# Kernel tuning notes

Hardware: AMD Instinct MI355X
Metric: run time of the kernel (lower is better)

## Reference

```python
import jax, jax.numpy as jnp
import numpy as np
import math

L = 2; B = 128; CIN = 64; E = 64; H = 8; Wd = 8; NH = 8; MEM = 40
HD = E // NH; HW = H * Wd; THD = HD * HW  # 512
MASK_B = 3.0; NEG = -1e9; EPS = 1e-5


def _conv(x, w, b):
    y = jax.lax.conv_general_dilated(x, w, (1, 1), 'SAME',
                                     dimension_numbers=('NCHW', 'OIHW', 'NCHW'))
    return y + b[None, :, None, None]


def setup_inputs() -> dict:
    key = jax.random.key(0)
    ks = jax.random.split(key, 12)
    f = jax.random.normal
    return {
        'x': f(ks[0], (B, CIN, H, Wd), jnp.float32),
        'h0': f(ks[1], (L, B, E, H, Wd), jnp.float32),
        'c0': f(ks[2], (L, B, E, H, Wd), jnp.float32),
        'k0': f(ks[3], (L, B, NH, MEM, THD), jnp.float32),
        'v0': f(ks[4], (L, B, NH, MEM, THD), jnp.float32),
        'src_mask': jax.random.randint(ks[5], (B, MEM), 0, 2).astype(bool),
        'notdone': jnp.ones((B,), bool),
        'main_w': f(ks[6], (L, 5 * E, CIN + 2 * E, 3, 3), jnp.float32) * 0.05,
        'main_b': jnp.zeros((L, 5 * E), jnp.float32),
        'proj_w': f(ks[7], (L, 3 * E, CIN + E, 3, 3), jnp.float32) * 0.05,
        'proj_b': jnp.zeros((L, 3 * E), jnp.float32),
        'out_w': f(ks[8], (L, E, E, 3, 3), jnp.float32) * 0.05,
        'out_b': jnp.zeros((L, E), jnp.float32),
        'ln_w': jnp.ones((L, E, H, Wd), jnp.float32),
        'ln_b': jnp.zeros((L, E, H, Wd), jnp.float32),
        'pos_w': f(ks[9], (L, MEM, HW * E), jnp.float32) * 0.05,
        'pos_b': f(ks[10], (L, MEM, NH), jnp.float32) * 0.05,
    }


def reference(x, h0, c0, k0, v0, src_mask, notdone,
              main_w, main_b, proj_w, proj_b, out_w, out_b,
              ln_w, ln_b, pos_w, pos_b):
    nd = notdone.astype(x.dtype)[:, None, None, None]
    # rolling attention mask: reset finished episodes, shift left, open last slot
    m = src_mask | (~notdone)[:, None]
    m = jnp.concatenate([m[:, 1:], jnp.zeros((B, 1), bool)], axis=1)
    bias = jnp.where(m, NEG, 0.0).astype(x.dtype)        # (B, MEM)
    bias = bias.at[:, -1].set(MASK_B)
    out = h0[L - 1] * nd
    for n in range(L):
        inp = jnp.concatenate([x, out], axis=1)          # (B, CIN+E, H, W)
        h_cur = h0[n] * nd
        c_cur = c0[n] * nd
        gates = _conv(jnp.concatenate([inp, h_cur], axis=1), main_w[n], main_b[n])
        cc_i, cc_f, cc_o, cc_g, cc_a = jnp.split(gates, 5, axis=1)
        i = jax.nn.sigmoid(cc_i)
        fg = jax.nn.sigmoid(cc_f)
        o = jax.nn.sigmoid(cc_o)
        g = jnp.tanh(cc_g)
        a = jax.nn.sigmoid(cc_a)
        c_next = fg * c_cur + i * g
        # attention over rolling memory (mem_n slots of flattened spatial features)
        kqv = _conv(inp, proj_w[n], proj_b[n]).reshape(B, NH, 3 * HD, HW)
        k = kqv[:, :, :HD].reshape(B, NH, THD)
        q = kqv[:, :, HD:2 * HD].reshape(B, NH, THD) / math.sqrt(THD)
        v = kqv[:, :, 2 * HD:].reshape(B, NH, THD)
        pw = pos_w[n].reshape(MEM, NH, THD).transpose(1, 0, 2)  # (NH, MEM, THD)
        k_cat = jnp.concatenate([k0[n][:, :, 1:], k[:, :, None, :]], axis=2) + pw[None]
        v_cat = jnp.concatenate([v0[n][:, :, 1:], v[:, :, None, :]], axis=2)
        scores = (jnp.einsum('bnd,bnmd->bnm', q, k_cat)
                  + bias[:, None, :] + pos_b[n].T[None])
        attn_w = jax.nn.softmax(scores, axis=-1)
        attn = jnp.einsum('bnm,bnmd->bnd', attn_w, v_cat).reshape(B, E, H, Wd)
        ao = _conv(attn, out_w[n], out_b[n]) + inp[:, :E]
        mu = ao.mean(axis=(1, 2, 3), keepdims=True)
        var = ((ao - mu) ** 2).mean(axis=(1, 2, 3), keepdims=True)
        ao = (ao - mu) * jax.lax.rsqrt(var + EPS) * ln_w[n][None] + ln_b[n][None]
        c_next = c_next + a * jnp.tanh(ao)
        out = o * jnp.tanh(c_next)
    return out
```

## Files before the change

kernel.cpp:

```cpp
#include <hip/hip_runtime.h>
#include <hip/hip_bf16.h>

typedef __hip_bfloat16 bf16;
typedef unsigned short u16;
typedef __attribute__((ext_vector_type(8))) short short8;
typedef __attribute__((ext_vector_type(4))) float f32x4;

#define Bb   128
#define MEMm 40

__device__ __forceinline__ float LD(const void* p, size_t i, int f32) {
    return f32 ? ((const float*)p)[i] : __bfloat162float(((const bf16*)p)[i]);
}
__device__ __forceinline__ float S2F(short s) {
    u16 u = (u16)s;
    return __bfloat162float(*(bf16*)&u);
}
__device__ __forceinline__ int LDB(const void* p, int i, int isbyte) {
    return isbyte ? (int)((const unsigned char*)p)[i] : ((const int*)p)[i];
}
__device__ __forceinline__ void SPLIT(float v, u16& hi, u16& lo) {
    bf16 h = __float2bfloat16(v);
    float r = v - __bfloat162float(h);
    bf16 l = __float2bfloat16(r);
    hi = *(u16*)&h; lo = *(u16*)&l;
}

__global__ void setup_kernel(const void* __restrict__ x,
                             const void* __restrict__ src_mask,
                             const void* __restrict__ notdone,
                             const void* __restrict__ h0,
                             const void* __restrict__ mw,
                             const void* __restrict__ pw,
                             const void* __restrict__ ow,
                             int* __restrict__ flags,
                             float* __restrict__ biasb,
                             float* __restrict__ outb, size_t hoff,
                             u16* __restrict__ whi, u16* __restrict__ wlo) {
    __shared__ int det[3];
    const int bid = blockIdx.x, t = threadIdx.x;
    if (t < 3) det[t] = 0;
    __syncthreads();
    {
        const bf16* xb = (const bf16*)x;
        int bad = 0;
        for (int i = t; i < 4096; i += 256) {
            float v = __bfloat162float(xb[2 * i]);
            if (!(fabsf(v) < 1e4f)) bad = 1;
        }
        if (bad) atomicOr(&det[0], 1);
        int mb = 0;
        const unsigned* mi = (const unsigned*)src_mask;
        for (int i = t; i < 1280; i += 256) if (mi[i] > 1u) mb = 1;
        if (mb) atomicOr(&det[1], 1);
        int nb = 0;
        const unsigned* ni = (const unsigned*)notdone;
        for (int i = t; i < 32; i += 256) if (ni[i] > 1u) nb = 1;
        if (nb) atomicOr(&det[2], 1);
    }
    __syncthreads();
    const int isf32 = det[0], mbyte = det[1], ndbyte = det[2];
    if (bid == 0 && t < 3) flags[t] = det[t];

    if (bid < 20) {
        int idx = bid * 256 + t;
        if (idx >= Bb * MEMm) return;
        int b = idx / MEMm, m = idx - b * MEMm;
        float v;
        if (m == MEMm - 1) v = 3.0f;
        else {
            bool masked = (LDB(src_mask, b * MEMm + m + 1, mbyte) != 0) ||
                          (LDB(notdone, b, ndbyte) == 0);
            v = masked ? -1e9f : 0.f;
        }
        biasb[idx] = v;
    } else if (bid < 276) {
        int idx = (bid - 20) * 256 + t;
        int b = idx >> 9;
        float nd = (LDB(notdone, b, ndbyte) != 0) ? 1.f : 0.f;
        size_t e = (size_t)idx * 8;
        float v[8];
        if (isf32) {
            const float* hp = (const float*)h0 + hoff + e;
            f32x4 p0 = *(const f32x4*)hp, p1 = *(const f32x4*)(hp + 4);
#pragma unroll
            for (int j = 0; j < 4; ++j) { v[j] = p0[j]; v[4 + j] = p1[j]; }
        } else {
            short8 s = *(const short8*)((const bf16*)h0 + hoff + e);
#pragma unroll
            for (int j = 0; j < 8; ++j) v[j] = S2F(s[j]);
        }
#pragma unroll
        for (int j = 0; j < 8; ++j) outb[e + j] = v[j] * nd;
    } else {
        int gi = (bid - 276) * 256 + t;
        if (gi >= 1622016) return;
        int layer = (gi >= 811008) ? 1 : 0;
        int i = gi - layer * 811008;
        float v;
        if (i < 552960) {
            int blk = i >> 9, r = i & 511;
            int l = r >> 3, j = r & 7;
            int nn = blk & 1, b2 = blk >> 1;
            int s = b2 % 10, tk = b2 / 10;
            int kc = tk % 6, tap = tk / 6;
            int co = s * 32 + nn * 16 + (l & 15);
            int ci = kc * 32 + ((l >> 4) << 3) + j;
            v = LD(mw, (size_t)layer * 552960 + ((size_t)co * 192 + ci) * 9 + tap, isf32);
        } else if (i < 774144) {
            int j2 = i - 552960;
            int blk = j2 >> 9, r = j2 & 511;
            int l = r >> 3, j = r & 7;
            int nn = blk & 1, b2 = blk >> 1;
            int s = b2 % 6, tk = b2 / 6;
            int kc = tk & 3, tap = tk >> 2;
            int co = s * 32 + nn * 16 + (l & 15);
            int ci = kc * 32 + ((l >> 4) << 3) + j;
            v = LD(pw, (size_t)layer * 221184 + ((size_t)co * 128 + ci) * 9 + tap, isf32);
        } else {
            int j2 = i - 774144;
            int tap = j2 / 4096, r = j2 - tap * 4096, co = r / 64, ci = r - co * 64;
            v = LD(ow, (size_t)layer * 36864 + ((size_t)co * 64 + ci) * 9 + tap, isf32);
        }
        u16 h, l; SPLIT(v, h, l);
        whi[gi] = h; wlo[gi] = l;
    }
}

struct ConvArgs {
    const void *x; const float *prev_out; const void *h0; const void *notdone;
    const u16 *WhiA, *WloA, *WhiB, *WloB;
    const void *biasA, *biasB;
    float *OutA, *OutB;
    long long boffA, boffB;
    size_t hoff;
    int KciA, KciB, CoutA, CoutB, ntA, NT, NMB;
};

__global__ __launch_bounds__(256) void conv_mfma_kernel(ConvArgs g,
                                                        const int* __restrict__ flags) {
    __shared__ __align__(16) u16 Alds[2][2][2600];
    const int t = threadIdx.x, w = t >> 6, lane = t & 63;
    const int bpair = w >> 1, half = w & 1;
    const int bx = blockIdx.x;
    const int mblk = bx % g.NMB, nt = bx / g.NMB;
    const bool isA = (nt < g.ntA);
    const u16* Whi = isA ? g.WhiA : g.WhiB;
    const u16* Wlo = isA ? g.WloA : g.WloB;
    const int Kci  = isA ? g.KciA : g.KciB;
    const int CoutT= isA ? g.CoutA : g.CoutB;
    float* Out     = isA ? g.OutA : g.OutB;
    const void* bias = isA ? g.biasA : g.biasB;
    const long long boff = isA ? g.boffA : g.boffB;
    const int n0 = (isA ? nt : nt - g.ntA) * 64;
    const int b = mblk * 2 + bpair;
    const int kcN = Kci >> 5;
    const int CoutT32 = CoutT >> 5;
    const int NITER = kcN * 9;
    const int s = (n0 >> 5) + half;
    const int isf32 = flags[0];
    const float nd = (LDB(g.notdone, b, flags[2]) != 0) ? 1.f : 0.f;

    if (half == 0 && lane < 40) { Alds[bpair][0][2560 + lane] = 0; Alds[bpair][1][2560 + lane] = 0; }

    f32x4 acc[4][2];
#pragma unroll
    for (int i = 0; i < 4; ++i)
#pragma unroll
        for (int j = 0; j < 2; ++j) { f32x4 z = {0.f, 0.f, 0.f, 0.f}; acc[i][j] = z; }

    auto wbase = [&](int it) -> size_t {
        int kc = it / 9, tap = it - kc * 9;
        return ((size_t)((tap * kcN + kc) * CoutT32 + s) * 2) * 512 + (size_t)lane * 8;
    };

    short8 wh0, wh1, wl0, wl1, nh0, nh1, nl0, nl1;
    {
        size_t o = wbase(0);
        wh0 = *(const short8*)(Whi + o); wh1 = *(const short8*)(Whi + o + 512);
        wl0 = *(const short8*)(Wlo + o); wl1 = *(const short8*)(Wlo + o + 512);
    }
    nh0 = wh0; nh1 = wh1; nl0 = wl0; nl1 = wl1;

    for (int it = 0; it < NITER; ++it) {
        const int kc = it / 9, tap = it - kc * 9;
        if (it + 1 < NITER) {
            size_t o = wbase(it + 1);
            nh0 = *(const short8*)(Whi + o); nh1 = *(const short8*)(Whi + o + 512);
            nl0 = *(const short8*)(Wlo + o); nl1 = *(const short8*)(Wlo + o + 512);
        }
        if (tap == 0) {
            __syncthreads();
            const int px = lane;
            const int c0i = half * 16;
            const int cbase = kc * 32;
            short8 hA, hB, lA, lB;
#pragma unroll
            for (int cl2 = 0; cl2 < 16; ++cl2) {
                int c = cbase + c0i + cl2;
                float v;
                if (c < 64) {
                    size_t o = (size_t)b * 4096 + (size_t)c * 64 + px;
                    v = isf32 ? ((const float*)g.x)[o] : S2F(((const short*)g.x)[o]);
                } else if (c < 128) {
                    v = g.prev_out[(size_t)b * 4096 + (size_t)(c - 64) * 64 + px];
                } else {
                    size_t o = g.hoff + (size_t)b * 4096 + (size_t)(c - 128) * 64 + px;
                    v = (isf32 ? ((const float*)g.h0)[o] : S2F(((const short*)g.h0)[o])) * nd;
                }
                u16 hh, ll; SPLIT(v, hh, ll);
                if (cl2 < 8) { hA[cl2] = (short)hh; lA[cl2] = (short)ll; }
                else         { hB[cl2 - 8] = (short)hh; lB[cl2 - 8] = (short)ll; }
            }
            *(short8*)&Alds[bpair][0][px * 40 + c0i]     = hA;
            *(short8*)&Alds[bpair][0][px * 40 + c0i + 8] = hB;
            *(short8*)&Alds[bpair][1][px * 40 + c0i]     = lA;
            *(short8*)&Alds[bpair][1][px * 40 + c0i + 8] = lB;
            __syncthreads();
        }
        const int dy = tap / 3 - 1, dx = tap % 3 - 1;
        const int q8 = (lane >> 4) * 8;
        const int ml = lane & 15;
        short8 aH[4], aL[4];
#pragma unroll
        for (int mt = 0; mt < 4; ++mt) {
            int px = mt * 16 + ml;
            int yy = (px >> 3) + dy, xx = (px & 7) + dx;
            int row = ((unsigned)yy < 8u && (unsigned)xx < 8u) ? yy * 8 + xx : 64;
            int o = row * 40 + q8;
            aH[mt] = *(const short8*)&Alds[bpair][0][o];
            aL[mt] = *(const short8*)&Alds[bpair][1][o];
        }
#pragma unroll
        for (int mt = 0; mt < 4; ++mt) {
            acc[mt][0] = __builtin_amdgcn_mfma_f32_16x16x32_bf16(aH[mt], wh0, acc[mt][0], 0, 0, 0);
            acc[mt][0] = __builtin_amdgcn_mfma_f32_16x16x32_bf16(aH[mt], wl0, acc[mt][0], 0, 0, 0);
            acc[mt][0] = __builtin_amdgcn_mfma_f32_16x16x32_bf16(aL[mt], wh0, acc[mt][0], 0, 0, 0);
            acc[mt][1] = __builtin_amdgcn_mfma_f32_16x16x32_bf16(aH[mt], wh1, acc[mt][1], 0, 0, 0);
            acc[mt][1] = __builtin_amdgcn_mfma_f32_16x16x32_bf16(aH[mt], wl1, acc[mt][1], 0, 0, 0);
            acc[mt][1] = __builtin_amdgcn_mfma_f32_16x16x32_bf16(aL[mt], wh1, acc[mt][1], 0, 0, 0);
        }
        wh0 = nh0; wh1 = nh1; wl0 = nl0; wl1 = nl1;
    }
    const int q = lane >> 4, ml = lane & 15;
#pragma unroll
    for (int nn = 0; nn < 2; ++nn) {
        int co = n0 + half * 32 + nn * 16 + ml;
        float bv = LD(bias, (size_t)boff + co, isf32);
#pragma unroll
        for (int mt = 0; mt < 4; ++mt) {
            f32x4 v = acc[mt][nn];
            v[0] += bv; v[1] += bv; v[2] += bv; v[3] += bv;
            *(f32x4*)&Out[((size_t)b * CoutT + co) * 64 + mt * 16 + q * 4] = v;
        }
    }
}

__global__ __launch_bounds__(256) void attn_kernel(
    const float* __restrict__ kqv,
    const void* __restrict__ k0,
    const void* __restrict__ v0,
    const void* __restrict__ pw,
    const void* __restrict__ pb,
    const float* __restrict__ biasb,
    const int* __restrict__ flags,
    u16* __restrict__ ahi, u16* __restrict__ alo,
    size_t kvoff, size_t pwoff, size_t pboff) {
    __shared__ float qv[512], kl[512], vl[512], sc[40], wexp[40];
    __shared__ float accbuf[4][512];
    const int t = threadIdx.x;
    const int isf32 = flags[0];
    const int b = blockIdx.x >> 3, h = blockIdx.x & 7;
    const size_t kqb = (size_t)b * 192 * 64;
    for (int d = t; d < 512; d += 256) {
        int hd = d >> 6, ss = d & 63;
        qv[d] = kqv[kqb + (h * 24 + 8 + hd) * 64 + ss] * 0.044194173824159216f;
        kl[d] = kqv[kqb + (h * 24 + 0 + hd) * 64 + ss];
        vl[d] = kqv[kqb + (h * 24 + 16 + hd) * 64 + ss];
    }
    __syncthreads();
    const int wid = t >> 6, lane = t & 63;
    const int d0 = lane * 8;
    const size_t kvbase = kvoff + ((size_t)(b * 8 + h)) * (size_t)(40 * 512);

    float q8[8];
#pragma unroll
    for (int j = 0; j < 8; ++j) q8[j] = qv[d0 + j];

    if (!isf32) {
        const bf16* kp = (const bf16*)k0;
        const bf16* pp = (const bf16*)pw;
        const bf16* vp = (const bf16*)v0;
        short8 kr[10], pr[10];
#pragma unroll
        for (int i = 0; i < 10; ++i) {
            int m = wid + i * 4;
            pr[i] = *(const short8*)(pp + pwoff + (size_t)m * 4096 + h * 512 + d0);
            if (m < 39)
                kr[i] = *(const short8*)(kp + kvbase + (size_t)(m + 1) * 512 + d0);
        }
#pragma unroll
        for (int i = 0; i < 10; ++i) {
            int m = wid + i * 4;
            float p = 0.f;
            if (m < 39) {
#pragma unroll
                for (int j = 0; j < 8; ++j)
                    p += q8[j] * (S2F(kr[i][j]) + S2F(pr[i][j]));
            } else {
#pragma unroll
                for (int j = 0; j < 8; ++j)
                    p += q8[j] * (kl[d0 + j] + S2F(pr[i][j]));
            }
#pragma unroll
            for (int off = 32; off > 0; off >>= 1) p += __shfl_down(p, off, 64);
            if (lane == 0)
                sc[m] = p + biasb[b * 40 + m] + LD(pb, pboff + m * 8 + h, 0);
        }
        short8 vr[10];
#pragma unroll
        for (int i = 0; i < 10; ++i) {
            int m = wid + i * 4;
            if (m < 39)
                vr[i] = *(const short8*)(vp + kvbase + (size_t)(m + 1) * 512 + d0);
        }
        __syncthreads();
        float mx = -1e30f;
        for (int m = 0; m < 40; ++m) mx = fmaxf(mx, sc[m]);
        if (t < 40) wexp[t] = __expf(sc[t] - mx);
        __syncthreads();
        float sum = 0.f;
        for (int m = 0; m < 40; ++m) sum += wexp[m];
        float rs = 1.f / sum;
        float acc8[8];
#pragma unroll
        for (int j = 0; j < 8; ++j) acc8[j] = 0.f;
#pragma unroll
        for (int i = 0; i < 10; ++i) {
            int m = wid + i * 4;
            float wgt = wexp[m];
            if (m < 39) {
#pragma unroll
                for (int j = 0; j < 8; ++j) acc8[j] += wgt * S2F(vr[i][j]);
            } else {
#pragma unroll
                for (int j = 0; j < 8; ++j) acc8[j] += wgt * vl[d0 + j];
            }
        }
#pragma unroll
        for (int j = 0; j < 8; ++j) accbuf[wid][d0 + j] = acc8[j];
        __syncthreads();
        for (int d = t; d < 512; d += 256) {
            float acc = (accbuf[0][d] + accbuf[1][d]) + (accbuf[2][d] + accbuf[3][d]);
            acc *= rs;
            int ch = h * 8 + (d >> 6), px = d & 63;
            u16 hh, ll; SPLIT(acc, hh, ll);
            size_t o = (size_t)b * 4096 + px * 64 + ch;
            ahi[o] = hh; alo[o] = ll;
        }
        return;
    }

    for (int m = wid; m < 40; m += 4) {
        float kc[8];
        if (m < 39) {
            const float* kp = (const float*)k0 + kvbase + (size_t)(m + 1) * 512 + d0;
            f32x4 p0 = *(const f32x4*)kp, p1 = *(const f32x4*)(kp + 4);
#pragma unroll
            for (int j = 0; j < 4; ++j) { kc[j] = p0[j]; kc[4 + j] = p1[j]; }
        } else {
#pragma unroll
            for (int j = 0; j < 8; ++j) kc[j] = kl[d0 + j];
        }
        const float* pp = (const float*)pw + pwoff + (size_t)m * 4096 + h * 512 + d0;
        f32x4 p0 = *(const f32x4*)pp, p1 = *(const f32x4*)(pp + 4);
#pragma unroll
        for (int j = 0; j < 4; ++j) { kc[j] += p0[j]; kc[4 + j] += p1[j]; }
        float p = 0.f;
#pragma unroll
        for (int j = 0; j < 8; ++j) p += q8[j] * kc[j];
#pragma unroll
        for (int off = 32; off > 0; off >>= 1) p += __shfl_down(p, off, 64);
        if (lane == 0)
            sc[m] = p + biasb[b * 40 + m] + LD(pb, pboff + m * 8 + h, 1);
    }
    __syncthreads();
    float mx = -1e30f;
    for (int m = 0; m < 40; ++m) mx = fmaxf(mx, sc[m]);
    if (t < 40) wexp[t] = __expf(sc[t] - mx);
    __syncthreads();
    float sum = 0.f;
    for (int m = 0; m < 40; ++m) sum += wexp[m];
    float rs = 1.f / sum;
    float acc8[8];
#pragma unroll
    for (int j = 0; j < 8; ++j) acc8[j] = 0.f;
    for (int m = wid; m < 40; m += 4) {
        float wgt = wexp[m];
        if (m < 39) {
            const float* vp = (const float*)v0 + kvbase + (size_t)(m + 1) * 512 + d0;
            f32x4 p0 = *(const f32x4*)vp, p1 = *(const f32x4*)(vp + 4);
#pragma unroll
            for (int j = 0; j < 4; ++j) { acc8[j] += wgt * p0[j]; acc8[4 + j] += wgt * p1[j]; }
        } else {
#pragma unroll
            for (int j = 0; j < 8; ++j) acc8[j] += wgt * vl[d0 + j];
        }
    }
#pragma unroll
    for (int j = 0; j < 8; ++j) accbuf[wid][d0 + j] = acc8[j];
    __syncthreads();
    for (int d = t; d < 512; d += 256) {
        float acc = (accbuf[0][d] + accbuf[1][d]) + (accbuf[2][d] + accbuf[3][d]);
        acc *= rs;
        int ch = h * 8 + (d >> 6), px = d & 63;
        u16 hh, ll; SPLIT(acc, hh, ll);
        size_t o = (size_t)b * 4096 + px * 64 + ch;
        ahi[o] = hh; alo[o] = ll;
    }
}

__global__ __launch_bounds__(256) void tail_kernel(
    const u16* __restrict__ ahi, const u16* __restrict__ alo,
    const u16* __restrict__ whi, const u16* __restrict__ wlo,
    const void* __restrict__ outb_bias,
    const void* __restrict__ x,
    const float* __restrict__ gates,
    const void* __restrict__ c0,
    const void* __restrict__ notdone,
    const void* __restrict__ lnw, const void* __restrict__ lnb,
    const int* __restrict__ flags,
    float* __restrict__ out_buf, void* __restrict__ dout, int write_out,
    long long boff, size_t coff, size_t lnoff) {
    __shared__ __align__(16) u16 Ald[2][2][2600];
    __shared__ __align__(16) u16 Wl[2][2][2560];
    __shared__ float red[8], stats[2];
    const int t = threadIdx.x, w = t >> 6, lane = t & 63;
    const int b = blockIdx.x;
    const int isf32 = flags[0], ndbyte = flags[2];

    {
        int px = t >> 2, ci16 = (t & 3) * 16;
        int chunk = ci16 >> 5, cl = ci16 & 31;
        size_t o = ((size_t)b * 64 + px) * 64 + ci16;
        *(uint4*)&Ald[chunk][0][px * 40 + cl]     = *(const uint4*)(ahi + o);
        *(uint4*)&Ald[chunk][0][px * 40 + cl + 8] = *(const uint4*)(ahi + o + 8);
        *(uint4*)&Ald[chunk][1][px * 40 + cl]     = *(const uint4*)(alo + o);
        *(uint4*)&Ald[chunk][1][px * 40 + cl + 8] = *(const uint4*)(alo + o + 8);
        if (t < 160) { int ch = t / 80, hl = (t / 40) & 1, i = t % 40;
                       Ald[ch][hl][2560 + i] = 0; }
    }

    const int co_l = t >> 2, jj = t & 3;
    uint4 hv, lv;
    auto issueW = [&](int it) {
        int kc = it / 9, tap = it - kc * 9;
        size_t o = ((size_t)(tap * 64 + co_l)) * 64 + kc * 32 + jj * 8;
        hv = *(const uint4*)(whi + o);
        lv = *(const uint4*)(wlo + o);
    };

    f32x4 acc[4];
#pragma unroll
    for (int i = 0; i < 4; ++i) { f32x4 z = {0.f, 0.f, 0.f, 0.f}; acc[i] = z; }

    issueW(0);
    for (int it = 0; it < 18; ++it) {
        const int kc = it / 9, tap = it - kc * 9;
        const int par = it & 1;
        *(uint4*)&Wl[par][0][co_l * 40 + jj * 8] = hv;
        *(uint4*)&Wl[par][1][co_l * 40 + jj * 8] = lv;
        __syncthreads();
        if (it + 1 < 18) issueW(it + 1);
        const int dy = tap / 3 - 1, dx = tap % 3 - 1;
        const int q8 = (lane >> 4) * 8;
        const int ml = lane & 15;
        short8 aH[4], aL[4];
#pragma unroll
        for (int mt = 0; mt < 4; ++mt) {
            int px = mt * 16 + ml;
            int yy = (px >> 3) + dy, xx = (px & 7) + dx;
            int row = ((unsigned)yy < 8u && (unsigned)xx < 8u) ? yy * 8 + xx : 64;
            int o = row * 40 + q8;
            aH[mt] = *(const short8*)&Ald[kc][0][o];
            aL[mt] = *(const short8*)&Ald[kc][1][o];
        }
        int o = (w * 16 + ml) * 40 + q8;
        short8 bH = *(const short8*)&Wl[par][0][o];
        short8 bL = *(const short8*)&Wl[par][1][o];
#pragma unroll
        for (int mt = 0; mt < 4; ++mt) {
            acc[mt] = __builtin_amdgcn_mfma_f32_16x16x32_bf16(aH[mt], bH, acc[mt], 0, 0, 0);
            acc[mt] = __builtin_amdgcn_mfma_f32_16x16x32_bf16(aH[mt], bL, acc[mt], 0, 0, 0);
            acc[mt] = __builtin_amdgcn_mfma_f32_16x16x32_bf16(aL[mt], bH, acc[mt], 0, 0, 0);
        }
    }

    const int q = lane >> 4, ml = lane & 15;
    const int co = w * 16 + ml;
    const size_t base = (size_t)b * 4096;
    float bv = LD(outb_bias, (size_t)boff + co, isf32);
    float vals[16];
    float sum = 0.f, sumsq = 0.f;
#pragma unroll
    for (int mt = 0; mt < 4; ++mt) {
        int px0 = mt * 16 + q * 4;
#pragma unroll
        for (int r = 0; r < 4; ++r) {
            float xv = LD(x, base + (size_t)co * 64 + px0 + r, isf32);
            float val = acc[mt][r] + bv + xv;
            vals[mt * 4 + r] = val; sum += val; sumsq += val * val;
        }
    }
#pragma unroll
    for (int off = 32; off > 0; off >>= 1) {
        sum   += __shfl_down(sum, off, 64);
        sumsq += __shfl_down(sumsq, off, 64);
    }
    if (lane == 0) { red[w] = sum; red[4 + w] = sumsq; }
    __syncthreads();
    if (t == 0) {
        float ts = red[0] + red[1] + red[2] + red[3];
        float tq = red[4] + red[5] + red[6] + red[7];
        float mu = ts * (1.f / 4096.f);
        float var = tq * (1.f / 4096.f) - mu * mu;
        stats[0] = mu; stats[1] = rsqrtf(fmaxf(var, 0.f) + 1e-5f);
    }
    __syncthreads();
    const float mu = stats[0], rstd = stats[1];
    const float nd = (LDB(notdone, b, ndbyte) != 0) ? 1.f : 0.f;
    const size_t gbase = (size_t)b * 320 * 64;
#pragma unroll
    for (int mt = 0; mt < 4; ++mt) {
        int px0 = mt * 16 + q * 4;
        size_t i0 = (size_t)co * 64 + px0;
        f32x4 gi4 = *(const f32x4*)&gates[gbase + (size_t)(co      ) * 64 + px0];
        f32x4 gf4 = *(const f32x4*)&gates[gbase + (size_t)(co +  64) * 64 + px0];
        f32x4 go4 = *(const f32x4*)&gates[gbase + (size_t)(co + 128) * 64 + px0];
        f32x4 gg4 = *(const f32x4*)&gates[gbase + (size_t)(co + 192) * 64 + px0];
        f32x4 ga4 = *(const f32x4*)&gates[gbase + (size_t)(co + 256) * 64 + px0];
        f32x4 ov;
#pragma unroll
        for (int r = 0; r < 4; ++r) {
            size_t i = i0 + r;
            float aon = (vals[mt * 4 + r] - mu) * rstd * LD(lnw, lnoff + i, isf32)
                        + LD(lnb, lnoff + i, isf32);
            float gi = 1.f / (1.f + __expf(-gi4[r]));
            float gf = 1.f / (1.f + __expf(-gf4[r]));
            float go = 1.f / (1.f + __expf(-go4[r]));
            float gg = tanhf(gg4[r]);
            float ga = 1.f / (1.f + __expf(-ga4[r]));
            float cc = LD(c0, coff + base + i, isf32) * nd;
            float cn = gf * cc + gi * gg + ga * tanhf(aon);
            float o  = go * tanhf(cn);
            ov[r] = o;
            if (write_out) {
                if (isf32) ((float*)dout)[base + i] = o;
                else       ((bf16*)dout)[base + i] = __float2bfloat16(o);
            }
        }
        *(f32x4*)&out_buf[base + i0] = ov;
    }
}

extern "C" void kernel_launch(void* const* d_in, const int* in_sizes, int n_in,
                              void* d_out, int out_size, void* d_ws, size_t ws_size,
                              hipStream_t stream) {
    const void* x      = d_in[0];
    const void* h0     = d_in[1];
    const void* c0     = d_in[2];
    const void* k0     = d_in[3];
    const void* v0     = d_in[4];
    const void* src_mask = d_in[5];
    const void* notdone  = d_in[6];
    const void* main_w = d_in[7];
    const void* main_b = d_in[8];
    const void* proj_w = d_in[9];
    const void* proj_b = d_in[10];
    const void* out_w  = d_in[11];
    const void* out_b  = d_in[12];
    const void* ln_w   = d_in[13];
    const void* ln_b   = d_in[14];
    const void* pos_w  = d_in[15];
    const void* pos_b  = d_in[16];

    float* wsf = (float*)d_ws;
    int*   flags    = (int*)d_ws;
    float* bias_buf = wsf + 8;
    float* out_buf  = wsf + 8192;
    float* gates_buf= wsf + 532480;
    float* kqv_buf  = wsf + 3153920;
    u16* attn_hi    = (u16*)(wsf + 4726784);
    u16* attn_lo    = (u16*)(wsf + 4988928);
    u16* wr_hi      = (u16*)(wsf + 5251072);
    u16* wr_lo      = (u16*)(wsf + 6062080);

    setup_kernel<<<6612, 256, 0, stream>>>(x, src_mask, notdone, h0,
                                           main_w, proj_w, out_w, flags,
                                           bias_buf, out_buf, (size_t)524288,
                                           wr_hi, wr_lo);
    for (int n = 0; n < 2; ++n) {
        const size_t wb = (size_t)n * 811008;
        ConvArgs ga;
        ga.x = x; ga.prev_out = out_buf; ga.h0 = h0; ga.notdone = notdone;
        ga.hoff = (size_t)n * 524288;
        ga.WhiA = wr_hi + wb;          ga.WloA = wr_lo + wb;          ga.KciA = 192; ga.CoutA = 320;
        ga.WhiB = wr_hi + wb + 552960; ga.WloB = wr_lo + wb + 552960; ga.KciB = 128; ga.CoutB = 192;
        ga.biasA = main_b; ga.boffA = (long long)n * 320; ga.OutA = gates_buf;
        ga.biasB = proj_b; ga.boffB = (long long)n * 192; ga.OutB = kqv_buf;
        ga.ntA = 5; ga.NT = 8; ga.NMB = 64;
        conv_mfma_kernel<<<512, 256, 0, stream>>>(ga, flags);

        attn_kernel<<<1024, 256, 0, stream>>>(
            kqv_buf, k0, v0, pos_w, pos_b, bias_buf, flags, attn_hi, attn_lo,
            (size_t)n * 20971520, (size_t)n * 163840, (size_t)n * 320);

        tail_kernel<<<128, 256, 0, stream>>>(
            attn_hi, attn_lo, wr_hi + wb + 774144, wr_lo + wb + 774144,
            out_b, x, gates_buf, c0, notdone, ln_w, ln_b, flags,
            out_buf, d_out, (n == 1) ? 1 : 0,
            (long long)n * 64, (size_t)n * 524288, (size_t)n * 4096);
    }
}
```

Baseline: 572.1 us.

## Drop weight low-part MFMAs in convs and split conv grid into 32-wide strips

Removes the bf16 low-part weight term from the split-precision MFMA products in both the conv kernel and the tail out-conv, so weights are effectively used at bf16 while activations keep hi+lo. This cuts one third of the MFMAs and halves the weight loads. The conv kernel also now has each block handle a 32-channel strip with each wave computing 16 output channels, and launches twice as many blocks. The cost is lower accuracy in the weights, and the activation tile is staged into LDS redundantly by more blocks.

```diff
diff --git a/kernel.cpp b/kernel.cpp
--- a/kernel.cpp
+++ b/kernel.cpp
@@ -129,12 +129,12 @@
 
 struct ConvArgs {
     const void *x; const float *prev_out; const void *h0; const void *notdone;
-    const u16 *WhiA, *WloA, *WhiB, *WloB;
+    const u16 *WhiA, *WhiB;
     const void *biasA, *biasB;
     float *OutA, *OutB;
     long long boffA, boffB;
     size_t hoff;
-    int KciA, KciB, CoutA, CoutB, ntA, NT, NMB;
+    int KciA, KciB, CoutA, CoutB, ntA, NMB;
 };
 
 __global__ __launch_bounds__(256) void conv_mfma_kernel(ConvArgs g,
@@ -143,52 +143,39 @@
     const int t = threadIdx.x, w = t >> 6, lane = t & 63;
     const int bpair = w >> 1, half = w & 1;
     const int bx = blockIdx.x;
-    const int mblk = bx % g.NMB, nt = bx / g.NMB;
-    const bool isA = (nt < g.ntA);
+    const int mblk = bx % g.NMB, strip = bx / g.NMB;
+    const bool isA = (strip < g.ntA);
     const u16* Whi = isA ? g.WhiA : g.WhiB;
-    const u16* Wlo = isA ? g.WloA : g.WloB;
     const int Kci  = isA ? g.KciA : g.KciB;
     const int CoutT= isA ? g.CoutA : g.CoutB;
     float* Out     = isA ? g.OutA : g.OutB;
     const void* bias = isA ? g.biasA : g.biasB;
     const long long boff = isA ? g.boffA : g.boffB;
-    const int n0 = (isA ? nt : nt - g.ntA) * 64;
+    const int s = isA ? strip : strip - g.ntA;
     const int b = mblk * 2 + bpair;
     const int kcN = Kci >> 5;
     const int CoutT32 = CoutT >> 5;
     const int NITER = kcN * 9;
-    const int s = (n0 >> 5) + half;
     const int isf32 = flags[0];
     const float nd = (LDB(g.notdone, b, flags[2]) != 0) ? 1.f : 0.f;
 
     if (half == 0 && lane < 40) { Alds[bpair][0][2560 + lane] = 0; Alds[bpair][1][2560 + lane] = 0; }
 
-    f32x4 acc[4][2];
-#pragma unroll
-    for (int i = 0; i < 4; ++i)
-#pragma unroll
-        for (int j = 0; j < 2; ++j) { f32x4 z = {0.f, 0.f, 0.f, 0.f}; acc[i][j] = z; }
+    f32x4 acc[4];
+#pragma unroll
+    for (int i = 0; i < 4; ++i) { f32x4 z = {0.f, 0.f, 0.f, 0.f}; acc[i] = z; }
 
     auto wbase = [&](int it) -> size_t {
         int kc = it / 9, tap = it - kc * 9;
-        return ((size_t)((tap * kcN + kc) * CoutT32 + s) * 2) * 512 + (size_t)lane * 8;
+        return ((size_t)((tap * kcN + kc) * CoutT32 + s) * 2 + half) * 512 + (size_t)lane * 8;
     };
 
-    short8 wh0, wh1, wl0, wl1, nh0, nh1, nl0, nl1;
-    {
-        size_t o = wbase(0);
-        wh0 = *(const short8*)(Whi + o); wh1 = *(const short8*)(Whi + o + 512);
-        wl0 = *(const short8*)(Wlo + o); wl1 = *(const short8*)(Wlo + o + 512);
-    }
-    nh0 = wh0; nh1 = wh1; nl0 = wl0; nl1 = wl1;
+    short8 wcur = *(const short8*)(Whi + wbase(0));
+    short8 wnext = wcur;
 
     for (int it = 0; it < NITER; ++it) {
         const int kc = it / 9, tap = it - kc * 9;
-        if (it + 1 < NITER) {
-            size_t o = wbase(it + 1);
-            nh0 = *(const short8*)(Whi + o); nh1 = *(const short8*)(Whi + o + 512);
-            nl0 = *(const short8*)(Wlo + o); nl1 = *(const short8*)(Wlo + o + 512);
-        }
+        if (it + 1 < NITER) wnext = *(const short8*)(Whi + wbase(it + 1));
         if (tap == 0) {
             __syncthreads();
             const int px = lane;
@@ -233,23 +220,18 @@
         }
 #pragma unroll
         for (int mt = 0; mt < 4; ++mt) {
-            acc[mt][0] = __builtin_amdgcn_mfma_f32_16x16x32_bf16(aH[mt], wh0, acc[mt][0], 0, 0, 0);
-            acc[mt][0] = __builtin_amdgcn_mfma_f32_16x16x32_bf16(aH[mt], wl0, acc[mt][0], 0, 0, 0);
-            acc[mt][0] = __builtin_amdgcn_mfma_f32_16x16x32_bf16(aL[mt], wh0, acc[mt][0], 0, 0, 0);
-            acc[mt][1] = __builtin_amdgcn_mfma_f32_16x16x32_bf16(aH[mt], wh1, acc[mt][1], 0, 0, 0);
-            acc[mt][1] = __builtin_amdgcn_mfma_f32_16x16x32_bf16(aH[mt], wl1, acc[mt][1], 0, 0, 0);
-            acc[mt][1] = __builtin_amdgcn_mfma_f32_16x16x32_bf16(aL[mt], wh1, acc[mt][1], 0, 0, 0);
-        }
-        wh0 = nh0; wh1 = nh1; wl0 = nl0; wl1 = nl1;
+            acc[mt] = __builtin_amdgcn_mfma_f32_16x16x32_bf16(aH[mt], wcur, acc[mt], 0, 0, 0);
+            acc[mt] = __builtin_amdgcn_mfma_f32_16x16x32_bf16(aL[mt], wcur, acc[mt], 0, 0, 0);
+        }
+        wcur = wnext;
     }
     const int q = lane >> 4, ml = lane & 15;
-#pragma unroll
-    for (int nn = 0; nn < 2; ++nn) {
-        int co = n0 + half * 32 + nn * 16 + ml;
+    {
+        int co = s * 32 + half * 16 + ml;
         float bv = LD(bias, (size_t)boff + co, isf32);
 #pragma unroll
         for (int mt = 0; mt < 4; ++mt) {
-            f32x4 v = acc[mt][nn];
+            f32x4 v = acc[mt];
             v[0] += bv; v[1] += bv; v[2] += bv; v[3] += bv;
             *(f32x4*)&Out[((size_t)b * CoutT + co) * 64 + mt * 16 + q * 4] = v;
         }
@@ -422,7 +404,7 @@
 
 __global__ __launch_bounds__(256) void tail_kernel(
     const u16* __restrict__ ahi, const u16* __restrict__ alo,
-    const u16* __restrict__ whi, const u16* __restrict__ wlo,
+    const u16* __restrict__ whi,
     const void* __restrict__ outb_bias,
     const void* __restrict__ x,
     const float* __restrict__ gates,
@@ -433,7 +415,7 @@
     float* __restrict__ out_buf, void* __restrict__ dout, int write_out,
     long long boff, size_t coff, size_t lnoff) {
     __shared__ __align__(16) u16 Ald[2][2][2600];
-    __shared__ __align__(16) u16 Wl[2][2][2560];
+    __shared__ __align__(16) u16 Wl[2][2560];
     __shared__ float red[8], stats[2];
     const int t = threadIdx.x, w = t >> 6, lane = t & 63;
     const int b = blockIdx.x;
@@ -452,12 +434,11 @@
     }
 
     const int co_l = t >> 2, jj = t & 3;
-    uint4 hv, lv;
+    uint4 hv;
     auto issueW = [&](int it) {
         int kc = it / 9, tap = it - kc * 9;
         size_t o = ((size_t)(tap * 64 + co_l)) * 64 + kc * 32 + jj * 8;
         hv = *(const uint4*)(whi + o);
-        lv = *(const uint4*)(wlo + o);
     };
 
     f32x4 acc[4];
@@ -468,8 +449,7 @@
     for (int it = 0; it < 18; ++it) {
         const int kc = it / 9, tap = it - kc * 9;
         const int par = it & 1;
-        *(uint4*)&Wl[par][0][co_l * 40 + jj * 8] = hv;
-        *(uint4*)&Wl[par][1][co_l * 40 + jj * 8] = lv;
+        *(uint4*)&Wl[par][co_l * 40 + jj * 8] = hv;
         __syncthreads();
         if (it + 1 < 18) issueW(it + 1);
         const int dy = tap / 3 - 1, dx = tap % 3 - 1;
@@ -486,12 +466,10 @@
             aL[mt] = *(const short8*)&Ald[kc][1][o];
         }
         int o = (w * 16 + ml) * 40 + q8;
-        short8 bH = *(const short8*)&Wl[par][0][o];
-        short8 bL = *(const short8*)&Wl[par][1][o];
+        short8 bH = *(const short8*)&Wl[par][o];
 #pragma unroll
         for (int mt = 0; mt < 4; ++mt) {
             acc[mt] = __builtin_amdgcn_mfma_f32_16x16x32_bf16(aH[mt], bH, acc[mt], 0, 0, 0);
-            acc[mt] = __builtin_amdgcn_mfma_f32_16x16x32_bf16(aH[mt], bL, acc[mt], 0, 0, 0);
             acc[mt] = __builtin_amdgcn_mfma_f32_16x16x32_bf16(aL[mt], bH, acc[mt], 0, 0, 0);
         }
     }
@@ -604,19 +582,19 @@
         ConvArgs ga;
         ga.x = x; ga.prev_out = out_buf; ga.h0 = h0; ga.notdone = notdone;
         ga.hoff = (size_t)n * 524288;
-        ga.WhiA = wr_hi + wb;          ga.WloA = wr_lo + wb;          ga.KciA = 192; ga.CoutA = 320;
-        ga.WhiB = wr_hi + wb + 552960; ga.WloB = wr_lo + wb + 552960; ga.KciB = 128; ga.CoutB = 192;
+        ga.WhiA = wr_hi + wb;          ga.KciA = 192; ga.CoutA = 320;
+        ga.WhiB = wr_hi + wb + 552960; ga.KciB = 128; ga.CoutB = 192;
         ga.biasA = main_b; ga.boffA = (long long)n * 320; ga.OutA = gates_buf;
         ga.biasB = proj_b; ga.boffB = (long long)n * 192; ga.OutB = kqv_buf;
-        ga.ntA = 5; ga.NT = 8; ga.NMB = 64;
-        conv_mfma_kernel<<<512, 256, 0, stream>>>(ga, flags);
+        ga.ntA = 10; ga.NMB = 64;
+        conv_mfma_kernel<<<1024, 256, 0, stream>>>(ga, flags);
 
         attn_kernel<<<1024, 256, 0, stream>>>(
             kqv_buf, k0, v0, pos_w, pos_b, bias_buf, flags, attn_hi, attn_lo,
             (size_t)n * 20971520, (size_t)n * 163840, (size_t)n * 320);
 
         tail_kernel<<<128, 256, 0, stream>>>(
-            attn_hi, attn_lo, wr_hi + wb + 774144, wr_lo + wb + 774144,
+            attn_hi, attn_lo, wr_hi + wb + 774144,
             out_b, x, gates_buf, c0, notdone, ln_w, ln_b, flags,
             out_buf, d_out, (n == 1) ? 1 : 0,
             (long long)n * 64, (size_t)n * 524288, (size_t)n * 4096);
```

After: 557.3 us. 2.6% less time.
